# Optimization experiments

Hardware: AMD Instinct MI355X
Metric: run time of the kernel (lower is better)

Reference implementation:

```python
import jax, jax.numpy as jnp
import numpy as np

N, C_IN, C_RED, H, W = 16, 256, 64, 48, 48


def conv1x1(x, w, b):
    # x: [N, Cin, H, W], w: [Cout, Cin], b: [Cout]
    return jnp.einsum('nchw,oc->nohw', x, w) + b[None, :, None, None]


def setup_inputs() -> dict:
    key = jax.random.key(0)
    ks = jax.random.split(key, 10)
    s_in = 1.0 / np.sqrt(C_IN)
    s_red = 1.0 / np.sqrt(C_RED)
    return {
        'feature_maps': jax.random.normal(ks[0], (N, C_IN, H, W), jnp.float32),
        'global_channel_output': jax.random.normal(ks[1], (N, C_IN, H, W), jnp.float32),
        'Wq': jax.random.uniform(ks[2], (C_RED, C_IN), jnp.float32, -s_in, s_in),
        'bq': jax.random.uniform(ks[3], (C_RED,), jnp.float32, -s_in, s_in),
        'Wk': jax.random.uniform(ks[4], (C_RED, C_IN), jnp.float32, -s_in, s_in),
        'bk': jax.random.uniform(ks[5], (C_RED,), jnp.float32, -s_in, s_in),
        'Wv': jax.random.uniform(ks[6], (C_RED, C_IN), jnp.float32, -s_in, s_in),
        'bv': jax.random.uniform(ks[7], (C_RED,), jnp.float32, -s_in, s_in),
        'Watt': jax.random.uniform(ks[8], (C_IN, C_RED), jnp.float32, -s_red, s_red),
        'batt': jax.random.uniform(ks[9], (C_IN,), jnp.float32, -s_red, s_red),
    }


def reference(feature_maps, global_channel_output, Wq, bq, Wk, bk, Wv, bv, Watt, batt):
    n, _, h, w = feature_maps.shape
    hw = h * w
    q = conv1x1(feature_maps, Wq, bq).reshape(n, -1, hw)   # [N, Cr, HW]
    k = conv1x1(feature_maps, Wk, bk).reshape(n, -1, hw)   # [N, Cr, HW]
    v = conv1x1(feature_maps, Wv, bv).reshape(n, -1, hw)   # [N, Cr, HW]
    # key^T @ query -> [N, HW, HW]
    qk = jnp.einsum('nci,ncj->nij', k, q)
    # global (flattened) softmax over the whole HWxHW matrix per batch element
    qk = jax.nn.softmax(qk.reshape(n, hw * hw), axis=-1).reshape(n, hw, hw)
    att = jnp.einsum('nci,nij->ncj', v, qk).reshape(n, -1, h, w)  # [N, Cr, H, W]
    att = conv1x1(att, Watt, batt)                                 # [N, Cin, H, W]
    return global_channel_output * att + global_channel_output
```

## Files before the change

kernel.cpp:

```cpp
#include <hip/hip_runtime.h>
#include <hip/hip_bf16.h>
#include <stdint.h>

#define NB   16
#define CIN  256
#define CRED 64
#define HW   2304
#define JT_ATT  128
#define NJT_ATT 18
#define NIG  4
#define NIT  9

typedef __bf16 bf16;
typedef __bf16 bf16x8 __attribute__((ext_vector_type(8)));
typedef __bf16 bf16x4 __attribute__((ext_vector_type(4)));
typedef float  f32x4  __attribute__((ext_vector_type(4)));

__global__ __launch_bounds__(256) void prep_kernel(
    const float* __restrict__ Wq, const float* __restrict__ bq,
    const float* __restrict__ Wk, const float* __restrict__ Wv,
    const float* __restrict__ Watt,
    bf16* __restrict__ Wqb, bf16* __restrict__ Wkb, bf16* __restrict__ Wvb,
    bf16* __restrict__ Wab, float* __restrict__ bqs)
{
    const float INVLN2 = 1.44269504088896f;
    int i = blockIdx.x * 256 + threadIdx.x;
    Wqb[i] = (bf16)(Wq[i] * INVLN2);
    Wkb[i] = (bf16)Wk[i];
    Wvb[i] = (bf16)Wv[i];
    Wab[i] = (bf16)Watt[i];
    if (i < CRED) bqs[i] = bq[i] * INVLN2;
}

__global__ __launch_bounds__(256) void qkv_kernel(
    const float* __restrict__ x,
    const bf16* __restrict__ Wqb, const float* __restrict__ bqs,
    const bf16* __restrict__ Wkb, const float* __restrict__ bk,
    const bf16* __restrict__ Wvb, const float* __restrict__ bv,
    bf16* __restrict__ qT, bf16* __restrict__ kT, bf16* __restrict__ v)
{
    __shared__ __align__(16) bf16 sX[32 * 264];
    const int jt = blockIdx.x, n = blockIdx.y;
    const int jbase = jt * 32;
    const int tid = threadIdx.x;
    const int lane = tid & 63, w = tid >> 6;
    const int l15 = lane & 15, q4 = lane >> 4;

    const float* xn = x + ((size_t)n * CIN) * HW + jbase;
    #pragma unroll
    for (int it = 0; it < 8; ++it) {
        int idx = tid + 256 * it;
        int c = idx >> 3, p4 = idx & 7;
        const float4 vv = *(const float4*)(xn + c * HW + p4 * 4);
        sX[(p4 * 4 + 0) * 264 + c] = (bf16)vv.x;
        sX[(p4 * 4 + 1) * 264 + c] = (bf16)vv.y;
        sX[(p4 * 4 + 2) * 264 + c] = (bf16)vv.z;
        sX[(p4 * 4 + 3) * 264 + c] = (bf16)vv.w;
    }
    __syncthreads();

    const bf16*  Ws[3] = {Wqb, Wkb, Wvb};
    const float* bs[3] = {bqs, bk, bv};
    #pragma unroll
    for (int wi = 0; wi < 3; ++wi) {
        bf16x8 a[8];
        const bf16* Wp = Ws[wi] + (w * 16 + l15) * CIN + q4 * 8;
        #pragma unroll
        for (int ks = 0; ks < 8; ++ks) a[ks] = *(const bf16x8*)(Wp + ks * 32);
        f32x4 acc[2] = {};
        #pragma unroll
        for (int nt = 0; nt < 2; ++nt) {
            #pragma unroll
            for (int ks = 0; ks < 8; ++ks) {
                bf16x8 b = *(const bf16x8*)(sX + (nt * 16 + l15) * 264 + ks * 32 + q4 * 8);
                acc[nt] = __builtin_amdgcn_mfma_f32_16x16x32_bf16(a[ks], b, acc[nt], 0, 0, 0);
            }
        }
        const int crb = w * 16 + q4 * 4;
        const float b0 = bs[wi][crb], b1 = bs[wi][crb + 1],
                    b2 = bs[wi][crb + 2], b3 = bs[wi][crb + 3];
        if (wi < 2) {
            bf16* dst = (wi == 0 ? qT : kT) + ((size_t)n * HW) * 64;
            #pragma unroll
            for (int nt = 0; nt < 2; ++nt) {
                int pos = jbase + nt * 16 + l15;
                bf16x4 pk = {(bf16)(acc[nt].x + b0), (bf16)(acc[nt].y + b1),
                             (bf16)(acc[nt].z + b2), (bf16)(acc[nt].w + b3)};
                *(bf16x4*)(dst + pos * 64 + crb) = pk;
            }
        } else {
            bf16* dst = v + ((size_t)n * CRED) * HW;
            #pragma unroll
            for (int nt = 0; nt < 2; ++nt) {
                int pos = jbase + nt * 16 + l15;
                dst[(crb + 0) * HW + pos] = (bf16)(acc[nt].x + b0);
                dst[(crb + 1) * HW + pos] = (bf16)(acc[nt].y + b1);
                dst[(crb + 2) * HW + pos] = (bf16)(acc[nt].z + b2);
                dst[(crb + 3) * HW + pos] = (bf16)(acc[nt].w + b3);
            }
        }
    }
}

__global__ __launch_bounds__(256, 4) void attn_kernel(
    const bf16* __restrict__ qT, const bf16* __restrict__ kT,
    const bf16* __restrict__ v,
    float* __restrict__ OTp, float* __restrict__ Z)
{
    __shared__ __align__(16) bf16 sK[2][64 * 72];
    __shared__ __align__(16) bf16 sV[2][64 * 72];
    const int jt = blockIdx.x, ig = blockIdx.y, n = blockIdx.z;
    const int jbase = jt * JT_ATT;
    const int tid = threadIdx.x;
    const int lane = tid & 63, w = tid >> 6;
    const int l15 = lane & 15, q4 = lane >> 4;

    bf16x8 qf[2][2];
    {
        const bf16* qn = qT + ((size_t)n * HW + jbase + w * 32) * 64;
        #pragma unroll
        for (int nt = 0; nt < 2; ++nt)
            #pragma unroll
            for (int ks = 0; ks < 2; ++ks)
                qf[nt][ks] = *(const bf16x8*)(qn + (nt * 16 + l15) * 64 + ks * 32 + q4 * 8);
    }

    f32x4 oacc[4][2] = {};
    float zacc = 0.f;
    const uint4* ksrc = (const uint4*)(kT + ((size_t)n * HW) * 64);
    const bf16* vbase = v + ((size_t)n * CRED) * HW;

    const int r0 = tid >> 3, c0 = tid & 7;
    const int ibase0 = ig * NIT * 64;
    const int pbase = ((c0 >> 2) & 1) * 32 + (c0 & 1) * 16 + ((c0 >> 1) & 1) * 4;

    uint4 kr0 = ksrc[(ibase0 + r0) * 8 + c0];
    uint4 kr1 = ksrc[(ibase0 + r0 + 32) * 8 + c0];
    uint4 vr0 = *(const uint4*)(vbase + (size_t)r0 * HW + ibase0 + c0 * 8);
    uint4 vr1 = *(const uint4*)(vbase + (size_t)(r0 + 32) * HW + ibase0 + c0 * 8);

    auto stage = [&](int buf) {
        uint4* dk = (uint4*)sK[buf];
        dk[r0 * 9 + c0] = kr0;
        dk[(r0 + 32) * 9 + c0] = kr1;
        bf16* dv0 = sV[buf] + r0 * 72 + pbase;
        bf16* dv1 = sV[buf] + (r0 + 32) * 72 + pbase;
        uint2 t;
        t.x = vr0.x; t.y = vr0.y; *(uint2*)(dv0)     = t;
        t.x = vr0.z; t.y = vr0.w; *(uint2*)(dv0 + 8) = t;
        t.x = vr1.x; t.y = vr1.y; *(uint2*)(dv1)     = t;
        t.x = vr1.z; t.y = vr1.w; *(uint2*)(dv1 + 8) = t;
    };

    stage(0);
    {
        const int nb = ibase0 + ((1 < NIT) ? 64 : 0);
        kr0 = ksrc[(nb + r0) * 8 + c0];
        kr1 = ksrc[(nb + r0 + 32) * 8 + c0];
        vr0 = *(const uint4*)(vbase + (size_t)r0 * HW + nb + c0 * 8);
        vr1 = *(const uint4*)(vbase + (size_t)(r0 + 32) * HW + nb + c0 * 8);
    }
    __syncthreads();

    for (int it = 0; it < NIT; ++it) {
        const int cur = it & 1;
        const bf16* K = sK[cur];
        const bf16* V = sV[cur];

        unsigned pw[2][4][2];
        #pragma unroll
        for (int is = 0; is < 4; ++is) {
            bf16x8 kf0 = *(const bf16x8*)(K + (is * 16 + l15) * 72 + q4 * 8);
            bf16x8 kf1 = *(const bf16x8*)(K + (is * 16 + l15) * 72 + 32 + q4 * 8);
            #pragma unroll
            for (int nt = 0; nt < 2; ++nt) {
                f32x4 s = {};
                s = __builtin_amdgcn_mfma_f32_16x16x32_bf16(kf0, qf[nt][0], s, 0, 0, 0);
                s = __builtin_amdgcn_mfma_f32_16x16x32_bf16(kf1, qf[nt][1], s, 0, 0, 0);
                float p0 = exp2f(s.x), p1 = exp2f(s.y);
                float p2 = exp2f(s.z), p3 = exp2f(s.w);
                zacc += (p0 + p1) + (p2 + p3);
                unsigned w0, w1;
                asm("v_cvt_pk_bf16_f32 %0, %1, %2" : "=v"(w0) : "v"(p0), "v"(p1));
                asm("v_cvt_pk_bf16_f32 %0, %1, %2" : "=v"(w1) : "v"(p2), "v"(p3));
                pw[nt][is][0] = w0;
                pw[nt][is][1] = w1;
            }
        }
        #pragma unroll
        for (int g = 0; g < 2; ++g) {
            bf16x8 vf[4];
            #pragma unroll
            for (int ct = 0; ct < 4; ++ct)
                vf[ct] = *(const bf16x8*)(V + (ct * 16 + l15) * 72 + g * 32 + q4 * 8);
            #pragma unroll
            for (int nt = 0; nt < 2; ++nt) {
                union { unsigned u[4]; bf16x8 v8; } pb;
                pb.u[0] = pw[nt][2 * g][0];
                pb.u[1] = pw[nt][2 * g][1];
                pb.u[2] = pw[nt][2 * g + 1][0];
                pb.u[3] = pw[nt][2 * g + 1][1];
                #pragma unroll
                for (int ct = 0; ct < 4; ++ct)
                    oacc[ct][nt] = __builtin_amdgcn_mfma_f32_16x16x32_bf16(
                        vf[ct], pb.v8, oacc[ct][nt], 0, 0, 0);
            }
        }

        if (it + 1 < NIT) {
            stage(cur ^ 1);
            const int nb = ibase0 + ((it + 2 < NIT) ? (it + 2) * 64 : 0);
            kr0 = ksrc[(nb + r0) * 8 + c0];
            kr1 = ksrc[(nb + r0 + 32) * 8 + c0];
            vr0 = *(const uint4*)(vbase + (size_t)r0 * HW + nb + c0 * 8);
            vr1 = *(const uint4*)(vbase + (size_t)(r0 + 32) * HW + nb + c0 * 8);
            __syncthreads();
        }
    }
    float* OTn = OTp + (((size_t)ig * NB + n) * HW) * 64;
    #pragma unroll
    for (int ct = 0; ct < 4; ++ct)
        #pragma unroll
        for (int nt = 0; nt < 2; ++nt) {
            int pos = jbase + w * 32 + nt * 16 + l15;
            *(f32x4*)(OTn + (size_t)pos * 64 + ct * 16 + q4 * 4) = oacc[ct][nt];
        }
    #pragma unroll
    for (int off = 32; off > 0; off >>= 1) zacc += __shfl_down(zacc, off);
    if (lane == 0) atomicAdd(Z + n, zacc);
}

__global__ __launch_bounds__(256) void out_kernel(
    const float* __restrict__ OTp, const float* __restrict__ Z,
    const bf16* __restrict__ Wab, const float* __restrict__ batt,
    const float* __restrict__ g, float* __restrict__ out)
{
    __shared__ __align__(16) bf16 sO[32 * 72];
    const int jt = blockIdx.x, n = blockIdx.y;
    const int jbase = jt * 32;
    const int tid = threadIdx.x;
    const int lane = tid & 63, w = tid >> 6;
    const int l15 = lane & 15, q4 = lane >> 4;
    const float invZ = 1.0f / Z[n];

    #pragma unroll
    for (int i0 = 0; i0 < 2; ++i0) {
        int i = tid + i0 * 256;
        int r = i >> 4, c4 = i & 15;
        const float* p = OTp + (((size_t)n * HW) + jbase + r) * 64 + c4 * 4;
        float4 s = *(const float4*)(p);
        #pragma unroll
        for (int igx = 1; igx < NIG; ++igx) {
            float4 t = *(const float4*)(p + (size_t)igx * NB * HW * 64);
            s.x += t.x; s.y += t.y; s.z += t.z; s.w += t.w;
        }
        bf16x4 pk = {(bf16)(s.x * invZ), (bf16)(s.y * invZ),
                     (bf16)(s.z * invZ), (bf16)(s.w * invZ)};
        *(bf16x4*)(sO + r * 72 + c4 * 4) = pk;
    }
    __syncthreads();

    bf16x8 bfr[2][2];
    #pragma unroll
    for (int nt = 0; nt < 2; ++nt)
        #pragma unroll
        for (int ks = 0; ks < 2; ++ks)
            bfr[nt][ks] = *(const bf16x8*)(sO + (nt * 16 + l15) * 72 + ks * 32 + q4 * 8);

    const float* gp = g + ((size_t)n * CIN) * HW;
    float* op = out + ((size_t)n * CIN) * HW;
    #pragma unroll
    for (int mt = 0; mt < 4; ++mt) {
        const bf16* Wp = Wab + (w * 64 + mt * 16 + l15) * 64 + q4 * 8;
        bf16x8 a0 = *(const bf16x8*)(Wp);
        bf16x8 a1 = *(const bf16x8*)(Wp + 32);
        const int co = w * 64 + mt * 16 + q4 * 4;
        const float c0 = batt[co], c1 = batt[co + 1], c2 = batt[co + 2], c3 = batt[co + 3];
        #pragma unroll
        for (int nt = 0; nt < 2; ++nt) {
            f32x4 acc = {};
            acc = __builtin_amdgcn_mfma_f32_16x16x32_bf16(a0, bfr[nt][0], acc, 0, 0, 0);
            acc = __builtin_amdgcn_mfma_f32_16x16x32_bf16(a1, bfr[nt][1], acc, 0, 0, 0);
            const int pos = jbase + nt * 16 + l15;
            const float g0 = gp[(co + 0) * HW + pos], g1 = gp[(co + 1) * HW + pos];
            const float g2 = gp[(co + 2) * HW + pos], g3 = gp[(co + 3) * HW + pos];
            op[(co + 0) * HW + pos] = g0 * (acc.x + c0 + 1.0f);
            op[(co + 1) * HW + pos] = g1 * (acc.y + c1 + 1.0f);
            op[(co + 2) * HW + pos] = g2 * (acc.z + c2 + 1.0f);
            op[(co + 3) * HW + pos] = g3 * (acc.w + c3 + 1.0f);
        }
    }
}

extern "C" void kernel_launch(void* const* d_in, const int* in_sizes, int n_in,
                              void* d_out, int out_size, void* d_ws, size_t ws_size,
                              hipStream_t stream) {
    const float* x    = (const float*)d_in[0];
    const float* g    = (const float*)d_in[1];
    const float* Wq   = (const float*)d_in[2];
    const float* bq   = (const float*)d_in[3];
    const float* Wk   = (const float*)d_in[4];
    const float* bk   = (const float*)d_in[5];
    const float* Wv   = (const float*)d_in[6];
    const float* bv   = (const float*)d_in[7];
    const float* Watt = (const float*)d_in[8];
    const float* batt = (const float*)d_in[9];
    float* out = (float*)d_out;

    char* ws = (char*)d_ws;
    const size_t qkv_sz = (size_t)NB * HW * CRED * sizeof(bf16);
    bf16*  qT  = (bf16*)(ws);
    bf16*  kT  = (bf16*)(ws + qkv_sz);
    bf16*  vv  = (bf16*)(ws + 2 * qkv_sz);
    float* OTp = (float*)(ws + 3 * qkv_sz);
    char*  w2  = ws + 3 * qkv_sz + (size_t)NIG * NB * HW * CRED * sizeof(float);
    float* Zp  = (float*)(w2);
    bf16*  Wqb = (bf16*)(w2 + 256);
    bf16*  Wkb = Wqb + CRED * CIN;
    bf16*  Wvb = Wkb + CRED * CIN;
    bf16*  Wab = Wvb + CRED * CIN;
    float* bqs = (float*)(Wab + CIN * CRED);

    hipMemsetAsync(Zp, 0, NB * sizeof(float), stream);

    dim3 blk(256);
    prep_kernel<<<dim3(64), blk, 0, stream>>>(Wq, bq, Wk, Wv, Watt, Wqb, Wkb, Wvb, Wab, bqs);
    qkv_kernel<<<dim3(HW / 32, NB), blk, 0, stream>>>(x, Wqb, bqs, Wkb, bk, Wvb, bv, qT, kT, vv);
    attn_kernel<<<dim3(NJT_ATT, NIG, NB), blk, 0, stream>>>(qT, kT, vv, OTp, Zp);
    out_kernel<<<dim3(HW / 32, NB), blk, 0, stream>>>(OTp, Zp, Wab, batt, g, out);
}
```

Measured before the change: 246.7 us.

## Halve attention i-splits, remap blocks across XCDs, coalesce V stores, add setprio

The attention kernel now splits the key dimension into 2 groups instead of 4, so each block runs 18 iterations. This halves the partial-output traffic but gives the grid half as many blocks (576 instead of 1152). The grid is flattened and remapped so consecutive virtual blocks land on the same XCD, which should improve L2 reuse of K/V for each batch. The qkv kernel packs pairs of channels into bf16x2 shared stores, and it stages V through shared memory so the global writes are coalesced 16-byte stores. The PV MFMA section is also wrapped in s_setprio to favour matrix issue.

```diff
diff --git a/kernel.cpp b/kernel.cpp
--- a/kernel.cpp
+++ b/kernel.cpp
@@ -8,12 +8,13 @@
 #define HW   2304
 #define JT_ATT  128
 #define NJT_ATT 18
-#define NIG  4
-#define NIT  9
+#define NIG  2
+#define NIT  18
 
 typedef __bf16 bf16;
 typedef __bf16 bf16x8 __attribute__((ext_vector_type(8)));
 typedef __bf16 bf16x4 __attribute__((ext_vector_type(4)));
+typedef __bf16 bf16x2 __attribute__((ext_vector_type(2)));
 typedef float  f32x4  __attribute__((ext_vector_type(4)));
 
 __global__ __launch_bounds__(256) void prep_kernel(
@@ -40,6 +41,7 @@
     bf16* __restrict__ qT, bf16* __restrict__ kT, bf16* __restrict__ v)
 {
     __shared__ __align__(16) bf16 sX[32 * 264];
+    __shared__ __align__(16) bf16 sVt[64 * 40];
     const int jt = blockIdx.x, n = blockIdx.y;
     const int jbase = jt * 32;
     const int tid = threadIdx.x;
@@ -48,14 +50,21 @@
 
     const float* xn = x + ((size_t)n * CIN) * HW + jbase;
     #pragma unroll
-    for (int it = 0; it < 8; ++it) {
+    for (int it = 0; it < 4; ++it) {
         int idx = tid + 256 * it;
-        int c = idx >> 3, p4 = idx & 7;
-        const float4 vv = *(const float4*)(xn + c * HW + p4 * 4);
-        sX[(p4 * 4 + 0) * 264 + c] = (bf16)vv.x;
-        sX[(p4 * 4 + 1) * 264 + c] = (bf16)vv.y;
-        sX[(p4 * 4 + 2) * 264 + c] = (bf16)vv.z;
-        sX[(p4 * 4 + 3) * 264 + c] = (bf16)vv.w;
+        int cp = idx >> 3, p4 = idx & 7;
+        const int c = cp * 2;
+        const float4 va = *(const float4*)(xn + (size_t)c * HW + p4 * 4);
+        const float4 vb = *(const float4*)(xn + (size_t)(c + 1) * HW + p4 * 4);
+        bf16x2 e0 = {(bf16)va.x, (bf16)vb.x};
+        bf16x2 e1 = {(bf16)va.y, (bf16)vb.y};
+        bf16x2 e2 = {(bf16)va.z, (bf16)vb.z};
+        bf16x2 e3 = {(bf16)va.w, (bf16)vb.w};
+        bf16* sp = sX + c;
+        *(bf16x2*)(sp + (p4 * 4 + 0) * 264) = e0;
+        *(bf16x2*)(sp + (p4 * 4 + 1) * 264) = e1;
+        *(bf16x2*)(sp + (p4 * 4 + 2) * 264) = e2;
+        *(bf16x2*)(sp + (p4 * 4 + 3) * 264) = e3;
     }
     __syncthreads();
 
@@ -89,16 +98,21 @@
                 *(bf16x4*)(dst + pos * 64 + crb) = pk;
             }
         } else {
-            bf16* dst = v + ((size_t)n * CRED) * HW;
             #pragma unroll
             for (int nt = 0; nt < 2; ++nt) {
-                int pos = jbase + nt * 16 + l15;
-                dst[(crb + 0) * HW + pos] = (bf16)(acc[nt].x + b0);
-                dst[(crb + 1) * HW + pos] = (bf16)(acc[nt].y + b1);
-                dst[(crb + 2) * HW + pos] = (bf16)(acc[nt].z + b2);
-                dst[(crb + 3) * HW + pos] = (bf16)(acc[nt].w + b3);
-            }
-        }
+                int pl = nt * 16 + l15;
+                sVt[(crb + 0) * 40 + pl] = (bf16)(acc[nt].x + b0);
+                sVt[(crb + 1) * 40 + pl] = (bf16)(acc[nt].y + b1);
+                sVt[(crb + 2) * 40 + pl] = (bf16)(acc[nt].z + b2);
+                sVt[(crb + 3) * 40 + pl] = (bf16)(acc[nt].w + b3);
+            }
+        }
+    }
+    __syncthreads();
+    {
+        const int cr = tid >> 2, p8 = (tid & 3) * 8;
+        uint4 val = *(const uint4*)(sVt + cr * 40 + p8);
+        *(uint4*)(v + ((size_t)n * CRED + cr) * HW + jbase + p8) = val;
     }
 }
 
@@ -109,7 +123,12 @@
 {
     __shared__ __align__(16) bf16 sK[2][64 * 72];
     __shared__ __align__(16) bf16 sV[2][64 * 72];
-    const int jt = blockIdx.x, ig = blockIdx.y, n = blockIdx.z;
+    const int phys = blockIdx.x;
+    const int virt = (phys & 7) * 72 + (phys >> 3);
+    const int n  = virt / (NJT_ATT * NIG);
+    const int r_ = virt % (NJT_ATT * NIG);
+    const int jt = r_ % NJT_ATT;
+    const int ig = r_ / NJT_ATT;
     const int jbase = jt * JT_ATT;
     const int tid = threadIdx.x;
     const int lane = tid & 63, w = tid >> 6;
@@ -154,7 +173,7 @@
 
     stage(0);
     {
-        const int nb = ibase0 + ((1 < NIT) ? 64 : 0);
+        const int nb = ibase0 + 64;
         kr0 = ksrc[(nb + r0) * 8 + c0];
         kr1 = ksrc[(nb + r0 + 32) * 8 + c0];
         vr0 = *(const uint4*)(vbase + (size_t)r0 * HW + nb + c0 * 8);
@@ -193,6 +212,7 @@
             #pragma unroll
             for (int ct = 0; ct < 4; ++ct)
                 vf[ct] = *(const bf16x8*)(V + (ct * 16 + l15) * 72 + g * 32 + q4 * 8);
+            __builtin_amdgcn_s_setprio(1);
             #pragma unroll
             for (int nt = 0; nt < 2; ++nt) {
                 union { unsigned u[4]; bf16x8 v8; } pb;
@@ -205,6 +225,7 @@
                     oacc[ct][nt] = __builtin_amdgcn_mfma_f32_16x16x32_bf16(
                         vf[ct], pb.v8, oacc[ct][nt], 0, 0, 0);
             }
+            __builtin_amdgcn_s_setprio(0);
         }
 
         if (it + 1 < NIT) {
@@ -326,6 +347,6 @@
     dim3 blk(256);
     prep_kernel<<<dim3(64), blk, 0, stream>>>(Wq, bq, Wk, Wv, Watt, Wqb, Wkb, Wvb, Wab, bqs);
     qkv_kernel<<<dim3(HW / 32, NB), blk, 0, stream>>>(x, Wqb, bqs, Wkb, bk, Wvb, bv, qT, kT, vv);
-    attn_kernel<<<dim3(NJT_ATT, NIG, NB), blk, 0, stream>>>(qT, kT, vv, OTp, Zp);
+    attn_kernel<<<dim3(NJT_ATT * NIG * NB), blk, 0, stream>>>(qT, kT, vv, OTp, Zp);
     out_kernel<<<dim3(HW / 32, NB), blk, 0, stream>>>(OTp, Zp, Wab, batt, g, out);
 }
```

Measured after the change: 225.5 us. 1.09x faster.
